# Performance work log

Hardware: AMD Instinct MI355X
Metric: run time of the kernel (lower is better)

The kernel has to match this reference:

```python
import jax, jax.numpy as jnp
import numpy as np

N_NODES = 50000
NEG_SLOPE = 0.2


def setup_inputs() -> dict:
    key = jax.random.key(0)
    k1, k2, k3, k4, k5 = jax.random.split(key, 5)
    in_c, out_c = 256, 256
    n_edges = 1_600_000
    x = jax.random.normal(k1, (N_NODES, in_c), dtype=jnp.float32)
    edge_index = jax.random.randint(k2, (2, n_edges), 0, N_NODES, dtype=jnp.int64)
    # Glorot-ish scaled params
    W = jax.random.normal(k3, (in_c, out_c), dtype=jnp.float32) * (1.0 / np.sqrt(in_c))
    att_src = jax.random.normal(k4, (out_c,), dtype=jnp.float32) * (1.0 / np.sqrt(out_c))
    att_dst = jax.random.normal(k5, (out_c,), dtype=jnp.float32) * (1.0 / np.sqrt(out_c))
    bias = jnp.zeros((out_c,), dtype=jnp.float32)
    return {"x": x, "edge_index": edge_index, "W": W, "att_src": att_src, "att_dst": att_dst, "bias": bias}


def reference(x, edge_index, W, att_src, att_dst, bias):
    N = x.shape[0]
    # PyG GATConv default: add self loops
    loops = jnp.arange(N, dtype=edge_index.dtype)
    src = jnp.concatenate([edge_index[0], loops])  # [E+N]
    dst = jnp.concatenate([edge_index[1], loops])  # [E+N]

    h = x @ W  # [N, out_c]
    a_s = h @ att_src  # [N] per-node source attention term
    a_d = h @ att_dst  # [N] per-node destination attention term

    e = a_s[src] + a_d[dst]  # [E+N]
    e = jnp.where(e > 0, e, NEG_SLOPE * e)  # LeakyReLU(0.2)

    # scatter-softmax over edges sharing a destination node
    e_max = jax.ops.segment_max(e, dst, num_segments=N)  # [N]
    e_exp = jnp.exp(e - e_max[dst])  # [E+N]
    denom = jax.ops.segment_sum(e_exp, dst, num_segments=N)  # [N]
    alpha = e_exp / denom[dst]  # [E+N]

    msgs = alpha[:, None] * h[src]  # [E+N, out_c]
    out = jax.ops.segment_sum(msgs, dst, num_segments=N)  # [N, out_c]
    return out + bias
```

## Files before the change

### kernel.cpp

```cpp
#include <hip/hip_runtime.h>
#include <math.h>

#define NODES_C 256
#define NEG_SLOPE 0.2f
#define CAP 128
#define NSLICE 8

typedef __attribute__((ext_vector_type(8))) short short8;
typedef __attribute__((ext_vector_type(4))) float f32x4;
typedef __attribute__((ext_vector_type(2))) float f32x2;
typedef __attribute__((ext_vector_type(4))) int i32x4;

__device__ inline unsigned short f2bf(float f) {
    unsigned u = __float_as_uint(f);
    u = (u + 0x7fff + ((u >> 16) & 1)) >> 16;
    return (unsigned short)u;
}
__device__ inline unsigned cvtpk_bf16(float a, float b) {
    unsigned r;
    asm("v_cvt_pk_bf16_f32 %0, %1, %2" : "=v"(r) : "v"(a), "v"(b));
    return r;
}
__device__ inline void gload_lds16(const void* g, void* l) {
    __builtin_amdgcn_global_load_lds(
        (const __attribute__((address_space(1))) unsigned int*)g,
        (__attribute__((address_space(3))) unsigned int*)l, 16, 0, 0);
}
__device__ inline void fma2(f32x2& a, unsigned u, float w) {
    f32x2 h;
    h.x = __uint_as_float(u << 16);
    h.y = __uint_as_float(u & 0xffff0000u);
    a += h * w;
}

__global__ __launch_bounds__(256) void k_init(const float* __restrict__ W,
                                              unsigned short* __restrict__ wt,
                                              uint4* __restrict__ zbase,
                                              int nZero4, int nbZero) {
    const int tid = threadIdx.x;
    int bid = blockIdx.x;
    if (bid < nbZero) {
        const int base = bid * 1024 + tid;
#pragma unroll
        for (int k = 0; k < 4; ++k) {
            const int i = base + k * 256;
            if (i < nZero4) zbase[i] = make_uint4(0, 0, 0, 0);
        }
        return;
    }
    bid -= nbZero;
    const int base = bid * 1024 + tid;
#pragma unroll
    for (int k = 0; k < 4; ++k) {
        const int i = base + k * 256;
        wt[i] = f2bf(W[(i & 255) * NODES_C + (i >> 8)]);
    }
}

__global__ __launch_bounds__(256) void k_stageB(
    const float* __restrict__ x, const unsigned short* __restrict__ wt,
    const float* __restrict__ att_src, const float* __restrict__ att_dst,
    unsigned short* __restrict__ hb, float* __restrict__ a_s, float* __restrict__ a_d,
    int n) {
    __shared__ unsigned short Ab[128 * 32];
    __shared__ unsigned short Bb[128 * 32];
    __shared__ float pfs[2][128], pfd[2][128];
    const int tid = threadIdx.x;
    const int lane = tid & 63;
    const int wid = tid >> 6;

    const int gbid = blockIdx.x;
    const int wr = wid >> 1, wc = wid & 1;
    const int brow = (gbid >> 1) * 128;
    const int bcol = (gbid & 1) * 128;
    const int rsel = lane & 15, ksel = (lane >> 4) * 8;

    f32x4 acc[4][4] = {};
    const int c0 = wid, c1 = wid + 4;
    const int srow0 = c0 * 16 + (lane >> 2), srow1 = c1 * 16 + (lane >> 2);
    const int sk = (lane & 3) * 8;
    const int arow = tid >> 1;
    const int kh = (tid & 1) * 16;
    const float4* xsrc = (const float4*)(x + (size_t)min(brow + arow, n - 1) * NODES_C);
    uint4* adst = (uint4*)&Ab[arow * 32 + kh];

    for (int kk = 0; kk < 256; kk += 32) {
        const int kb = (kk + kh) >> 2;
        const float4 v0 = xsrc[kb + 0];
        const float4 v1 = xsrc[kb + 1];
        const float4 v2 = xsrc[kb + 2];
        const float4 v3 = xsrc[kb + 3];
        gload_lds16(wt + (size_t)(bcol + srow0) * NODES_C + kk + sk, Bb + c0 * 512);
        gload_lds16(wt + (size_t)(bcol + srow1) * NODES_C + kk + sk, Bb + c1 * 512);
        adst[0] = make_uint4(cvtpk_bf16(v0.x, v0.y), cvtpk_bf16(v0.z, v0.w),
                             cvtpk_bf16(v1.x, v1.y), cvtpk_bf16(v1.z, v1.w));
        adst[1] = make_uint4(cvtpk_bf16(v2.x, v2.y), cvtpk_bf16(v2.z, v2.w),
                             cvtpk_bf16(v3.x, v3.y), cvtpk_bf16(v3.z, v3.w));
        __syncthreads();
        short8 afrag[4], bfrag[4];
#pragma unroll
        for (int m = 0; m < 4; ++m)
            afrag[m] = *(const short8*)&Ab[(wr * 64 + m * 16 + rsel) * 32 + ksel];
#pragma unroll
        for (int q = 0; q < 4; ++q)
            bfrag[q] = *(const short8*)&Bb[(wc * 64 + q * 16 + rsel) * 32 + ksel];
#pragma unroll
        for (int m = 0; m < 4; ++m)
#pragma unroll
            for (int q = 0; q < 4; ++q)
                acc[m][q] = __builtin_amdgcn_mfma_f32_16x16x32_bf16(bfrag[q], afrag[m], acc[m][q], 0, 0, 0);
        __syncthreads();
    }

    const int xr = lane & 15;
    const int cg = (lane >> 4) * 4;
    float4 avs4[4], avd4[4];
#pragma unroll
    for (int q = 0; q < 4; ++q) {
        avs4[q] = *(const float4*)&att_src[bcol + wc * 64 + q * 16 + cg];
        avd4[q] = *(const float4*)&att_dst[bcol + wc * 64 + q * 16 + cg];
    }
#pragma unroll
    for (int m = 0; m < 4; ++m) {
        const int rloc = wr * 64 + m * 16 + xr;
        const int r = brow + rloc;
        float s = 0.f, d = 0.f;
#pragma unroll
        for (int q = 0; q < 4; ++q) {
            const f32x4 v = acc[m][q];
            s += v[0] * avs4[q].x + v[1] * avs4[q].y + v[2] * avs4[q].z + v[3] * avs4[q].w;
            d += v[0] * avd4[q].x + v[1] * avd4[q].y + v[2] * avd4[q].z + v[3] * avd4[q].w;
            if (r < n) {
                const uint2 hv = make_uint2(cvtpk_bf16(v[0], v[1]), cvtpk_bf16(v[2], v[3]));
                *(uint2*)&hb[(size_t)r * NODES_C + bcol + wc * 64 + q * 16 + cg] = hv;
            }
        }
        s += __shfl_xor(s, 16); s += __shfl_xor(s, 32);
        d += __shfl_xor(d, 16); d += __shfl_xor(d, 32);
        if (lane < 16) { pfs[wc][rloc] = s; pfd[wc][rloc] = d; }
    }
    __syncthreads();
    if (tid < 128) {
        const int r = brow + tid;
        if (r < n) atomicAdd(&a_s[r], pfs[0][tid] + pfs[1][tid]);
    } else {
        const int t2 = tid - 128;
        const int r = brow + t2;
        if (r < n) atomicAdd(&a_d[r], pfd[0][t2] + pfd[1][t2]);
    }
}

__global__ __launch_bounds__(256) void k_permute(const int* __restrict__ src,
                                                 const int* __restrict__ dst,
                                                 const float* __restrict__ a_s,
                                                 const float* __restrict__ a_d,
                                                 int* __restrict__ cnt,
                                                 unsigned* __restrict__ sedge,
                                                 int E4, int bps, int nsNode, int n) {
    const int slice = blockIdx.x & (NSLICE - 1);
    const int j = blockIdx.x >> 3;
    const int lo = slice * nsNode;
    const int hi = min(lo + nsNode, n);
    const int stride = bps * 256;
    const i32x4* d4 = (const i32x4*)dst;
    const i32x4* s4 = (const i32x4*)src;

    for (int g = j * 256 + threadIdx.x; g < E4; g += stride) {
        const i32x4 dv = __builtin_nontemporal_load(&d4[g]);
        const bool m0 = (dv.x >= lo) & (dv.x < hi);
        const bool m1 = (dv.y >= lo) & (dv.y < hi);
        const bool m2 = (dv.z >= lo) & (dv.z < hi);
        const bool m3 = (dv.w >= lo) & (dv.w < hi);
        if (!(m0 | m1 | m2 | m3)) continue;
        const i32x4 sv = __builtin_nontemporal_load(&s4[g]);
#pragma unroll
        for (int k = 0; k < 4; ++k) {
            const bool mk = k == 0 ? m0 : k == 1 ? m1 : k == 2 ? m2 : m3;
            if (!mk) continue;
            const int d = k == 0 ? dv.x : k == 1 ? dv.y : k == 2 ? dv.z : dv.w;
            const int s = k == 0 ? sv.x : k == 1 ? sv.y : k == 2 ? sv.z : sv.w;
            float e = a_s[s] + a_d[d];
            e = e > 0.f ? e : NEG_SLOPE * e;
            const float w = __expf(e);
            const int pos = atomicAdd(&cnt[d], 1);
            if (pos < CAP) sedge[(d << 7) + pos] = ((unsigned)f2bf(w) << 16) | (unsigned)s;
        }
    }
}

__global__ __launch_bounds__(256) void k_gather(const int* __restrict__ cnt,
                                                const unsigned* __restrict__ sedge,
                                                const unsigned short* __restrict__ hb,
                                                const float* __restrict__ a_s,
                                                const float* __restrict__ a_d,
                                                const float* __restrict__ bias,
                                                float* __restrict__ out, int n) {
    const int node = (int)((blockIdx.x * (size_t)blockDim.x + threadIdx.x) >> 6);
    const int lane = threadIdx.x & 63;
    if (node >= n) return;
    const int c = min(__builtin_amdgcn_readfirstlane(cnt[node]), CAP);
    const int base = node << 7;
    const int hf = lane >> 5, q = lane & 31;
    const uint4* hrow = (const uint4*)hb;

    float eself = a_s[node] + a_d[node];
    eself = eself > 0.f ? eself : NEG_SLOPE * eself;
    const unsigned selfmeta = ((unsigned)f2bf(__expf(eself)) << 16) | (unsigned)node;
    const int items = c + 1;

    f32x2 acc0 = {0.f, 0.f}, acc1 = {0.f, 0.f}, acc2 = {0.f, 0.f}, acc3 = {0.f, 0.f};
    float dsum = 0.f;

    int it = 0;
    for (; it + 16 <= c; it += 16) {
        const int bi = __builtin_amdgcn_readfirstlane(base + it);
        const uint4 pA = *(const uint4*)&sedge[bi];
        const uint4 pB = *(const uint4*)&sedge[bi + 4];
        const uint4 pC = *(const uint4*)&sedge[bi + 8];
        const uint4 pD = *(const uint4*)&sedge[bi + 12];
        const unsigned m0 = hf ? pA.y : pA.x;
        const unsigned m1 = hf ? pA.w : pA.z;
        const unsigned m2 = hf ? pB.y : pB.x;
        const unsigned m3 = hf ? pB.w : pB.z;
        const unsigned m4 = hf ? pC.y : pC.x;
        const unsigned m5 = hf ? pC.w : pC.z;
        const unsigned m6 = hf ? pD.y : pD.x;
        const unsigned m7 = hf ? pD.w : pD.z;
        const uint4 r0 = hrow[(size_t)(m0 & 0xffffu) * 32 + q];
        const uint4 r1 = hrow[(size_t)(m1 & 0xffffu) * 32 + q];
        const uint4 r2 = hrow[(size_t)(m2 & 0xffffu) * 32 + q];
        const uint4 r3 = hrow[(size_t)(m3 & 0xffffu) * 32 + q];
        const uint4 r4 = hrow[(size_t)(m4 & 0xffffu) * 32 + q];
        const uint4 r5 = hrow[(size_t)(m5 & 0xffffu) * 32 + q];
        const uint4 r6 = hrow[(size_t)(m6 & 0xffffu) * 32 + q];
        const uint4 r7 = hrow[(size_t)(m7 & 0xffffu) * 32 + q];
        float w;
        w = __uint_as_float(m0 & 0xffff0000u); dsum += w;
        fma2(acc0, r0.x, w); fma2(acc1, r0.y, w); fma2(acc2, r0.z, w); fma2(acc3, r0.w, w);
        w = __uint_as_float(m1 & 0xffff0000u); dsum += w;
        fma2(acc0, r1.x, w); fma2(acc1, r1.y, w); fma2(acc2, r1.z, w); fma2(acc3, r1.w, w);
        w = __uint_as_float(m2 & 0xffff0000u); dsum += w;
        fma2(acc0, r2.x, w); fma2(acc1, r2.y, w); fma2(acc2, r2.z, w); fma2(acc3, r2.w, w);
        w = __uint_as_float(m3 & 0xffff0000u); dsum += w;
        fma2(acc0, r3.x, w); fma2(acc1, r3.y, w); fma2(acc2, r3.z, w); fma2(acc3, r3.w, w);
        w = __uint_as_float(m4 & 0xffff0000u); dsum += w;
        fma2(acc0, r4.x, w); fma2(acc1, r4.y, w); fma2(acc2, r4.z, w); fma2(acc3, r4.w, w);
        w = __uint_as_float(m5 & 0xffff0000u); dsum += w;
        fma2(acc0, r5.x, w); fma2(acc1, r5.y, w); fma2(acc2, r5.z, w); fma2(acc3, r5.w, w);
        w = __uint_as_float(m6 & 0xffff0000u); dsum += w;
        fma2(acc0, r6.x, w); fma2(acc1, r6.y, w); fma2(acc2, r6.z, w); fma2(acc3, r6.w, w);
        w = __uint_as_float(m7 & 0xffff0000u); dsum += w;
        fma2(acc0, r7.x, w); fma2(acc1, r7.y, w); fma2(acc2, r7.z, w); fma2(acc3, r7.w, w);
    }
    for (; it < items; it += 2) {
        const int bi = __builtin_amdgcn_readfirstlane(base + it);
        const unsigned t0 = (it     < c) ? sedge[bi]     : ((it     == c) ? selfmeta : 0u);
        const unsigned t1 = (it + 1 < c) ? sedge[bi + 1] : ((it + 1 == c) ? selfmeta : 0u);
        const unsigned m = hf ? t1 : t0;
        const uint4 r = hrow[(size_t)(m & 0xffffu) * 32 + q];
        const float w = __uint_as_float(m & 0xffff0000u);
        dsum += w;
        fma2(acc0, r.x, w); fma2(acc1, r.y, w);
        fma2(acc2, r.z, w); fma2(acc3, r.w, w);
    }

    dsum += __shfl_xor(dsum, 32);
    acc0.x += __shfl_xor(acc0.x, 32); acc0.y += __shfl_xor(acc0.y, 32);
    acc1.x += __shfl_xor(acc1.x, 32); acc1.y += __shfl_xor(acc1.y, 32);
    acc2.x += __shfl_xor(acc2.x, 32); acc2.y += __shfl_xor(acc2.y, 32);
    acc3.x += __shfl_xor(acc3.x, 32); acc3.y += __shfl_xor(acc3.y, 32);

    const float inv = 1.f / dsum;
    const f32x2 A = hf ? acc2 : acc0;
    const f32x2 B = hf ? acc3 : acc1;
    const int ch = q * 8 + hf * 4;
    const float4 b4 = *(const float4*)&bias[ch];
    float4 o;
    o.x = fmaf(A.x, inv, b4.x);
    o.y = fmaf(A.y, inv, b4.y);
    o.z = fmaf(B.x, inv, b4.z);
    o.w = fmaf(B.y, inv, b4.w);
    *(float4*)&out[(size_t)node * NODES_C + ch] = o;
}

extern "C" void kernel_launch(void* const* d_in, const int* in_sizes, int n_in,
                              void* d_out, int out_size, void* d_ws, size_t ws_size,
                              hipStream_t stream) {
    const float* x       = (const float*)d_in[0];
    const int*   edge    = (const int*)d_in[1];
    const float* W       = (const float*)d_in[2];
    const float* att_src = (const float*)d_in[3];
    const float* att_dst = (const float*)d_in[4];
    const float* bias    = (const float*)d_in[5];
    float* out = (float*)d_out;

    const int n = in_sizes[0] / NODES_C;
    const int E = in_sizes[1] / 2;
    const int Mpad = (n + 127) & ~127;
    const int* src = edge;
    const int* dst = edge + E;

    char* p = (char*)d_ws;
    auto carve = [&p](size_t bytes) { char* r = p; p += (bytes + 255) & ~(size_t)255; return r; };
    unsigned short* wt = (unsigned short*)carve((size_t)NODES_C * NODES_C * 2);
    unsigned short* hb = (unsigned short*)carve((size_t)n * NODES_C * 2);
    float* a_s = (float*)carve((size_t)n * 4 * 3);
    float* a_d = a_s + n;
    int*   cnt = (int*)(a_d + n);
    unsigned* sedge = (unsigned*)carve((size_t)n * CAP * 4);

    const int nZero4 = (n * 3) / 4;
    const int nbZero = (nZero4 + 1023) / 1024;
    const int nbCvtw = (NODES_C * NODES_C) / 1024;

    k_init<<<nbZero + nbCvtw, 256, 0, stream>>>(W, wt, (uint4*)a_s, nZero4, nbZero);
    k_stageB<<<(Mpad / 128) * 2, 256, 0, stream>>>(
        x, wt, att_src, att_dst, hb, a_s, a_d, n);

    const int E4 = E / 4;
    const int bps = 192;
    const int nsNode = (n + NSLICE - 1) / NSLICE;
    k_permute<<<bps * NSLICE, 256, 0, stream>>>(src, dst, a_s, a_d, cnt, sedge,
                                                E4, bps, nsNode, n);
    k_gather<<<(n + 3) / 4, 256, 0, stream>>>(cnt, sedge, hb, a_s, a_d, bias, out, n);
}
```

Measured before the change: 227.3 us.

## Widen GEMM K-tile with swizzled LDS, XCD-aware block remap, unroll edge permute

After: 229.1 us. About the same (+0.8%).

```diff
diff --git a/kernel.cpp b/kernel.cpp
--- a/kernel.cpp
+++ b/kernel.cpp
@@ -32,6 +32,7 @@
     h.y = __uint_as_float(u & 0xffff0000u);
     a += h * w;
 }
+__device__ inline int swz(int row, int e) { return e ^ ((row & 7) << 3); }
 
 __global__ __launch_bounds__(256) void k_init(const float* __restrict__ W,
                                               unsigned short* __restrict__ wt,
@@ -62,53 +63,70 @@
     const float* __restrict__ att_src, const float* __restrict__ att_dst,
     unsigned short* __restrict__ hb, float* __restrict__ a_s, float* __restrict__ a_d,
     int n) {
-    __shared__ unsigned short Ab[128 * 32];
-    __shared__ unsigned short Bb[128 * 32];
+    __shared__ unsigned short Ab[128 * 64];
+    __shared__ unsigned short Bb[128 * 64];
     __shared__ float pfs[2][128], pfd[2][128];
     const int tid = threadIdx.x;
     const int lane = tid & 63;
     const int wid = tid >> 6;
 
-    const int gbid = blockIdx.x;
+    const int nwg = (int)gridDim.x;
+    const int q8 = nwg >> 3, r8 = nwg & 7;
+    const int xcd = blockIdx.x & 7, jj = blockIdx.x >> 3;
+    const int t = (xcd < r8 ? xcd * (q8 + 1) : r8 * (q8 + 1) + (xcd - r8) * q8) + jj;
+
     const int wr = wid >> 1, wc = wid & 1;
-    const int brow = (gbid >> 1) * 128;
-    const int bcol = (gbid & 1) * 128;
+    const int brow = (t >> 1) * 128;
+    const int bcol = (t & 1) * 128;
     const int rsel = lane & 15, ksel = (lane >> 4) * 8;
 
     f32x4 acc[4][4] = {};
-    const int c0 = wid, c1 = wid + 4;
-    const int srow0 = c0 * 16 + (lane >> 2), srow1 = c1 * 16 + (lane >> 2);
-    const int sk = (lane & 3) * 8;
+
+    const int bc0 = wid * 4;
+    const int srB = lane >> 3;
+    const int gcB = swz(srB, (lane & 7) * 8);
     const int arow = tid >> 1;
-    const int kh = (tid & 1) * 16;
+    const int kh = (tid & 1) * 32;
     const float4* xsrc = (const float4*)(x + (size_t)min(brow + arow, n - 1) * NODES_C);
-    uint4* adst = (uint4*)&Ab[arow * 32 + kh];
-
-    for (int kk = 0; kk < 256; kk += 32) {
+
+    for (int kk = 0; kk < 256; kk += 64) {
         const int kb = (kk + kh) >> 2;
-        const float4 v0 = xsrc[kb + 0];
-        const float4 v1 = xsrc[kb + 1];
-        const float4 v2 = xsrc[kb + 2];
-        const float4 v3 = xsrc[kb + 3];
-        gload_lds16(wt + (size_t)(bcol + srow0) * NODES_C + kk + sk, Bb + c0 * 512);
-        gload_lds16(wt + (size_t)(bcol + srow1) * NODES_C + kk + sk, Bb + c1 * 512);
-        adst[0] = make_uint4(cvtpk_bf16(v0.x, v0.y), cvtpk_bf16(v0.z, v0.w),
-                             cvtpk_bf16(v1.x, v1.y), cvtpk_bf16(v1.z, v1.w));
-        adst[1] = make_uint4(cvtpk_bf16(v2.x, v2.y), cvtpk_bf16(v2.z, v2.w),
-                             cvtpk_bf16(v3.x, v3.y), cvtpk_bf16(v3.z, v3.w));
+        float4 v[8];
+#pragma unroll
+        for (int i = 0; i < 8; ++i) v[i] = xsrc[kb + i];
+#pragma unroll
+        for (int c = 0; c < 4; ++c) {
+            const int ch = bc0 + c;
+            gload_lds16(wt + (size_t)(bcol + ch * 8 + srB) * NODES_C + kk + gcB,
+                        Bb + ch * 512);
+        }
+#pragma unroll
+        for (int i = 0; i < 4; ++i)
+            *(uint4*)&Ab[arow * 64 + swz(arow, kh + 8 * i)] =
+                make_uint4(cvtpk_bf16(v[2 * i].x, v[2 * i].y),
+                           cvtpk_bf16(v[2 * i].z, v[2 * i].w),
+                           cvtpk_bf16(v[2 * i + 1].x, v[2 * i + 1].y),
+                           cvtpk_bf16(v[2 * i + 1].z, v[2 * i + 1].w));
         __syncthreads();
-        short8 afrag[4], bfrag[4];
-#pragma unroll
-        for (int m = 0; m < 4; ++m)
-            afrag[m] = *(const short8*)&Ab[(wr * 64 + m * 16 + rsel) * 32 + ksel];
-#pragma unroll
-        for (int q = 0; q < 4; ++q)
-            bfrag[q] = *(const short8*)&Bb[(wc * 64 + q * 16 + rsel) * 32 + ksel];
-#pragma unroll
-        for (int m = 0; m < 4; ++m)
-#pragma unroll
-            for (int q = 0; q < 4; ++q)
-                acc[m][q] = __builtin_amdgcn_mfma_f32_16x16x32_bf16(bfrag[q], afrag[m], acc[m][q], 0, 0, 0);
+#pragma unroll
+        for (int ks = 0; ks < 64; ks += 32) {
+            short8 afrag[4], bfrag[4];
+#pragma unroll
+            for (int m = 0; m < 4; ++m) {
+                const int r = wr * 64 + m * 16 + rsel;
+                afrag[m] = *(const short8*)&Ab[r * 64 + swz(r, ksel + ks)];
+            }
+#pragma unroll
+            for (int q = 0; q < 4; ++q) {
+                const int r = wc * 64 + q * 16 + rsel;
+                bfrag[q] = *(const short8*)&Bb[r * 64 + swz(r, ksel + ks)];
+            }
+#pragma unroll
+            for (int m = 0; m < 4; ++m)
+#pragma unroll
+                for (int q = 0; q < 4; ++q)
+                    acc[m][q] = __builtin_amdgcn_mfma_f32_16x16x32_bf16(bfrag[q], afrag[m], acc[m][q], 0, 0, 0);
+        }
         __syncthreads();
     }
 
@@ -165,25 +183,51 @@
     const i32x4* d4 = (const i32x4*)dst;
     const i32x4* s4 = (const i32x4*)src;
 
-    for (int g = j * 256 + threadIdx.x; g < E4; g += stride) {
-        const i32x4 dv = __builtin_nontemporal_load(&d4[g]);
-        const bool m0 = (dv.x >= lo) & (dv.x < hi);
-        const bool m1 = (dv.y >= lo) & (dv.y < hi);
-        const bool m2 = (dv.z >= lo) & (dv.z < hi);
-        const bool m3 = (dv.w >= lo) & (dv.w < hi);
-        if (!(m0 | m1 | m2 | m3)) continue;
-        const i32x4 sv = __builtin_nontemporal_load(&s4[g]);
-#pragma unroll
-        for (int k = 0; k < 4; ++k) {
-            const bool mk = k == 0 ? m0 : k == 1 ? m1 : k == 2 ? m2 : m3;
-            if (!mk) continue;
-            const int d = k == 0 ? dv.x : k == 1 ? dv.y : k == 2 ? dv.z : dv.w;
-            const int s = k == 0 ? sv.x : k == 1 ? sv.y : k == 2 ? sv.z : sv.w;
-            float e = a_s[s] + a_d[d];
-            e = e > 0.f ? e : NEG_SLOPE * e;
-            const float w = __expf(e);
-            const int pos = atomicAdd(&cnt[d], 1);
-            if (pos < CAP) sedge[(d << 7) + pos] = ((unsigned)f2bf(w) << 16) | (unsigned)s;
+    for (int g = j * 256 + threadIdx.x; g < E4; g += 2 * stride) {
+        const int g2 = g + stride;
+        const bool has2 = g2 < E4;
+        const i32x4 dvA = __builtin_nontemporal_load(&d4[g]);
+        i32x4 dvB = {lo - 1, lo - 1, lo - 1, lo - 1};
+        if (has2) dvB = __builtin_nontemporal_load(&d4[g2]);
+
+        const bool a0 = (dvA.x >= lo) & (dvA.x < hi);
+        const bool a1 = (dvA.y >= lo) & (dvA.y < hi);
+        const bool a2 = (dvA.z >= lo) & (dvA.z < hi);
+        const bool a3 = (dvA.w >= lo) & (dvA.w < hi);
+        const bool b0 = (dvB.x >= lo) & (dvB.x < hi);
+        const bool b1 = (dvB.y >= lo) & (dvB.y < hi);
+        const bool b2 = (dvB.z >= lo) & (dvB.z < hi);
+        const bool b3 = (dvB.w >= lo) & (dvB.w < hi);
+
+        if (a0 | a1 | a2 | a3) {
+            const i32x4 sv = __builtin_nontemporal_load(&s4[g]);
+#pragma unroll
+            for (int k = 0; k < 4; ++k) {
+                const bool mk = k == 0 ? a0 : k == 1 ? a1 : k == 2 ? a2 : a3;
+                if (!mk) continue;
+                const int d = k == 0 ? dvA.x : k == 1 ? dvA.y : k == 2 ? dvA.z : dvA.w;
+                const int s = k == 0 ? sv.x : k == 1 ? sv.y : k == 2 ? sv.z : sv.w;
+                float e = a_s[s] + a_d[d];
+                e = e > 0.f ? e : NEG_SLOPE * e;
+                const float w = __expf(e);
+                const int pos = atomicAdd(&cnt[d], 1);
+                if (pos < CAP) sedge[(d << 7) + pos] = ((unsigned)f2bf(w) << 16) | (unsigned)s;
+            }
+        }
+        if (b0 | b1 | b2 | b3) {
+            const i32x4 sv = __builtin_nontemporal_load(&s4[g2]);
+#pragma unroll
+            for (int k = 0; k < 4; ++k) {
+                const bool mk = k == 0 ? b0 : k == 1 ? b1 : k == 2 ? b2 : b3;
+                if (!mk) continue;
+                const int d = k == 0 ? dvB.x : k == 1 ? dvB.y : k == 2 ? dvB.z : dvB.w;
+                const int s = k == 0 ? sv.x : k == 1 ? sv.y : k == 2 ? sv.z : sv.w;
+                float e = a_s[s] + a_d[d];
+                e = e > 0.f ? e : NEG_SLOPE * e;
+                const float w = __expf(e);
+                const int pos = atomicAdd(&cnt[d], 1);
+                if (pos < CAP) sedge[(d << 7) + pos] = ((unsigned)f2bf(w) << 16) | (unsigned)s;
+            }
         }
     }
 }
```
